# Kernel optimization log

Measured on AMD Instinct MI355X. Metric: run time of the kernel, lower is better.

Reference implementation:

```python
import jax, jax.numpy as jnp
import numpy as np

V, T, D, L, H, F = 32000, 1024, 768, 8, 12, 3072
DH = D // H
SCALE = 1.0 / np.sqrt(DH)
EPS = 1e-5


def layer_norm(x, w, b):
    mu = jnp.mean(x, axis=-1, keepdims=True)
    var = jnp.mean(jnp.square(x - mu), axis=-1, keepdims=True)
    return (x - mu) * jax.lax.rsqrt(var + EPS) * w + b


def setup_inputs() -> dict:
    key = jax.random.key(0)
    ks = jax.random.split(key, 10)
    def nrm(k, shape, std=0.02):
        return (jax.random.normal(k, shape, dtype=jnp.float32) * std)
    inp = {
        "idx": jax.random.randint(ks[0], (4, T), 0, V, dtype=jnp.int32),
        "targets": jax.random.randint(ks[1], (4, T), 0, V, dtype=jnp.int32),
        "tok_emb": nrm(ks[2], (V, D)),
        "pos_emb": nrm(ks[3], (T, D)),
        "qkv_w": nrm(ks[4], (L, 3 * D, D)),
        "qkv_b": jnp.zeros((L, 3 * D), jnp.float32),
        "proj_w": nrm(ks[5], (L, D, D)),
        "proj_b": jnp.zeros((L, D), jnp.float32),
        "fc1_w": nrm(ks[6], (L, F, D)),
        "fc1_b": jnp.zeros((L, F), jnp.float32),
        "fc2_w": nrm(ks[7], (L, D, F)),
        "fc2_b": jnp.zeros((L, D), jnp.float32),
        "ln1_w": jnp.ones((L, D), jnp.float32),
        "ln1_b": jnp.zeros((L, D), jnp.float32),
        "ln2_w": jnp.ones((L, D), jnp.float32),
        "ln2_b": jnp.zeros((L, D), jnp.float32),
        "lnf_w": jnp.ones((D,), jnp.float32),
        "lnf_b": jnp.zeros((D,), jnp.float32),
    }
    return inp


def gpt_forward(idx, targets, tok_emb, pos_emb, qkv_w, qkv_b, proj_w, proj_b,
                fc1_w, fc1_b, fc2_w, fc2_b, ln1_w, ln1_b, ln2_w, ln2_b, lnf_w, lnf_b):
    B, Tc = idx.shape
    x = tok_emb[idx] + pos_emb[:Tc][None]  # [B,T,D]
    causal = jnp.tril(jnp.ones((Tc, Tc), bool))

    def block(x, p):
        qw, qb, pw, pb, f1w, f1b, f2w, f2b, l1w, l1b, l2w, l2b = p
        h = layer_norm(x, l1w, l1b)
        qkv = h @ qw.T + qb  # [B,T,3D]
        q, k, v = jnp.split(qkv, 3, axis=-1)
        q = q.reshape(B, Tc, H, DH).transpose(0, 2, 1, 3)  # [B,H,T,DH]
        k = k.reshape(B, Tc, H, DH).transpose(0, 2, 1, 3)
        v = v.reshape(B, Tc, H, DH).transpose(0, 2, 1, 3)
        att = jnp.einsum('bhqd,bhkd->bhqk', q, k) * SCALE
        att = jnp.where(causal, att, -jnp.inf)
        att = jax.nn.softmax(att, axis=-1)
        y = jnp.einsum('bhqk,bhkd->bhqd', att, v)
        y = y.transpose(0, 2, 1, 3).reshape(B, Tc, D)
        x = x + y @ pw.T + pb
        h2 = layer_norm(x, l2w, l2b)
        x = x + jax.nn.gelu(h2 @ f1w.T + f1b, approximate=False) @ f2w.T + f2b
        return x, None

    x, _ = jax.lax.scan(block, x, (qkv_w, qkv_b, proj_w, proj_b,
                                   fc1_w, fc1_b, fc2_w, fc2_b,
                                   ln1_w, ln1_b, ln2_w, ln2_b))
    x = layer_norm(x, lnf_w, lnf_b)
    logits = jnp.einsum('btd,vd->btv', x, tok_emb)  # tied lm_head, output_mult=1
    logp = jax.nn.log_softmax(logits, axis=-1)
    valid = targets != -100
    tgt = jnp.where(valid, targets, 0)
    nll = -jnp.take_along_axis(logp, tgt[..., None], axis=-1)[..., 0]
    loss = jnp.sum(nll * valid) / jnp.maximum(jnp.sum(valid), 1)
    return logits, loss


def reference(idx, targets, tok_emb, pos_emb, qkv_w, qkv_b, proj_w, proj_b,
              fc1_w, fc1_b, fc2_w, fc2_b, ln1_w, ln1_b, ln2_w, ln2_b, lnf_w, lnf_b):
    return gpt_forward(idx, targets, tok_emb, pos_emb, qkv_w, qkv_b, proj_w, proj_b,
                       fc1_w, fc1_b, fc2_w, fc2_b, ln1_w, ln1_b, ln2_w, ln2_b, lnf_w, lnf_b)
```

## Files before the change

kernel.cpp:

```cpp
#include <hip/hip_runtime.h>
#include <hip/hip_bf16.h>
#include <math.h>

#define BATCH 4
#define T 1024
#define D 768
#define L 8
#define H 12
#define F 3072
#define V 32000
#define DH 64
#define M (BATCH*T)
#define D3 (3*D)
#define SCALE 0.125f
#define VCHUNK 6400
#define PBT 125

typedef unsigned short u16;
typedef __attribute__((ext_vector_type(8))) short bf16x8;
typedef __attribute__((ext_vector_type(4))) float f32x4;

__device__ inline u16 f2b(float f) {
  __hip_bfloat16 h = __float2bfloat16(f);
  return *(u16*)&h;
}

__device__ inline void gll16(const void* g, void* l) {
  __builtin_amdgcn_global_load_lds(
      (const __attribute__((address_space(1))) unsigned int*)g,
      (__attribute__((address_space(3))) unsigned int*)l, 16, 0, 0);
}

__device__ inline int swzi(int r, int c) {
  return (r * 64 + c) ^ ((((r & 7) ^ ((r >> 3) & 7))) << 3);
}

__device__ inline float block_reduce(float v, bool is_max, float* buf4) {
  int lane = threadIdx.x & 63, wid = threadIdx.x >> 6;
#pragma unroll
  for (int off = 32; off; off >>= 1) {
    float o = __shfl_down(v, off, 64);
    v = is_max ? fmaxf(v, o) : v + o;
  }
  if (lane == 0) buf4[wid] = v;
  __syncthreads();
  float r = is_max ? fmaxf(fmaxf(buf4[0], buf4[1]), fmaxf(buf4[2], buf4[3]))
                   : buf4[0] + buf4[1] + buf4[2] + buf4[3];
  __syncthreads();
  return r;
}

__global__ __launch_bounds__(256) void k_embed(const int* __restrict__ idx,
                                               const float* __restrict__ tok,
                                               const float* __restrict__ pos,
                                               float* __restrict__ x) {
  int i = blockIdx.x * 256 + threadIdx.x;
  int row = i / D, d = i - row * D;
  int t = row & (T - 1);
  x[i] = tok[(size_t)idx[row] * D + d] + pos[(size_t)t * D + d];
}

__global__ __launch_bounds__(256) void k_cvt(const float* __restrict__ in,
                                             u16* __restrict__ out, int n4) {
  int i = blockIdx.x * 256 + threadIdx.x;
  if (i >= n4) return;
  float4 v = ((const float4*)in)[i];
  ushort4 o;
  o.x = f2b(v.x); o.y = f2b(v.y); o.z = f2b(v.z); o.w = f2b(v.w);
  ((ushort4*)out)[i] = o;
}

__global__ __launch_bounds__(256) void k_cvtw(const float* __restrict__ q,
                                              const float* __restrict__ p,
                                              const float* __restrict__ f1,
                                              const float* __restrict__ f2,
                                              u16* __restrict__ out) {
  const int N0 = L * D3 * D / 4, N1 = L * D * D / 4;
  const int N2 = L * F * D / 4, N3 = L * D * F / 4;
  int i = blockIdx.x * 256 + threadIdx.x;
  if (i >= N0 + N1 + N2 + N3) return;
  const float* src;
  int j = i;
  if (i < N0) { src = q; }
  else if (i < N0 + N1) { src = p; j = i - N0; }
  else if (i < N0 + N1 + N2) { src = f1; j = i - N0 - N1; }
  else { src = f2; j = i - N0 - N1 - N2; }
  float4 v = ((const float4*)src)[j];
  ushort4 o;
  o.x = f2b(v.x); o.y = f2b(v.y); o.z = f2b(v.z); o.w = f2b(v.w);
  ((ushort4*)out)[i] = o;
}

__global__ __launch_bounds__(256) void k_lnorm(const float* __restrict__ x,
                                               const float* __restrict__ w,
                                               const float* __restrict__ b,
                                               u16* __restrict__ out) {
  int lane = threadIdx.x & 63, wid = threadIdx.x >> 6;
  int row = blockIdx.x * 4 + wid;
  const float4* xr = (const float4*)(x + (size_t)row * D);
  float4 v[3];
  float s = 0.f, ss = 0.f;
#pragma unroll
  for (int p = 0; p < 3; ++p) {
    v[p] = xr[lane + 64 * p];
    s += v[p].x + v[p].y + v[p].z + v[p].w;
    ss += v[p].x * v[p].x + v[p].y * v[p].y + v[p].z * v[p].z + v[p].w * v[p].w;
  }
#pragma unroll
  for (int off = 32; off; off >>= 1) {
    s += __shfl_xor(s, off, 64);
    ss += __shfl_xor(ss, off, 64);
  }
  float mu = s * (1.0f / D);
  float var = ss * (1.0f / D) - mu * mu;
  float rs = rsqrtf(var + 1e-5f);
  ushort4* orow = (ushort4*)(out + (size_t)row * D);
#pragma unroll
  for (int p = 0; p < 3; ++p) {
    float4 wv = ((const float4*)w)[lane + 64 * p];
    float4 bv = ((const float4*)b)[lane + 64 * p];
    ushort4 o;
    o.x = f2b((v[p].x - mu) * rs * wv.x + bv.x);
    o.y = f2b((v[p].y - mu) * rs * wv.y + bv.y);
    o.z = f2b((v[p].z - mu) * rs * wv.z + bv.z);
    o.w = f2b((v[p].w - mu) * rs * wv.w + bv.w);
    orow[lane + 64 * p] = o;
  }
}

__global__ __launch_bounds__(512, 2) void k_gemm8(
    const u16* __restrict__ A, const u16* __restrict__ W,
    const float* __restrict__ bias, const float* __restrict__ resid,
    void* __restrict__ Cout, int K, int ldC, int flags) {
  __shared__ __attribute__((aligned(16))) u16 lds[2][2][128 * 64];
  int tid = threadIdx.x, w = tid >> 6, lane = tid & 63;
  int wm = w >> 2, wn = w & 3;
  int bn = blockIdx.x, bm = blockIdx.y;
  int frow = lane & 15, g = lane >> 4;
  int sr = lane >> 3, scu = lane & 7;
  const u16* Ab = A + (size_t)bm * 128 * K;
  const u16* Wb = W + (size_t)bn * 128 * K;
  int NT = K >> 6;

  f32x4 acc[4][2];
#pragma unroll
  for (int i = 0; i < 4; ++i)
#pragma unroll
    for (int j = 0; j < 2; ++j) acc[i][j] = (f32x4)(0.f);

#define STG(t)                                                            \
  {                                                                       \
    _Pragma("unroll") for (int rr = 0; rr < 2; ++rr) {                    \
      int row = rr * 64 + w * 8 + sr;                                     \
      int gcu = scu ^ (row & 7);                                          \
      gll16(Ab + (size_t)row * K + (t) * 64 + gcu * 8,                    \
            &lds[(t) & 1][0][(rr * 64 + w * 8) * 64]);                    \
      gll16(Wb + (size_t)row * K + (t) * 64 + gcu * 8,                    \
            &lds[(t) & 1][1][(rr * 64 + w * 8) * 64]);                    \
    }                                                                     \
  }

  STG(0);
  asm volatile("s_waitcnt vmcnt(0)");
  __builtin_amdgcn_s_barrier();

  for (int t = 0; t < NT; ++t) {
    if (t + 1 < NT) {
      STG(t + 1);
      asm volatile("s_waitcnt vmcnt(4)");
    } else {
      asm volatile("s_waitcnt vmcnt(0)");
    }
    __builtin_amdgcn_s_barrier();
    const u16* bA = &lds[t & 1][0][0];
    const u16* bB = &lds[t & 1][1][0];
    bf16x8 ar[8], br[4];
#pragma unroll
    for (int i = 0; i < 4; ++i)
#pragma unroll
      for (int kk = 0; kk < 2; ++kk) {
        int r = wm * 64 + i * 16 + frow;
        ar[i * 2 + kk] = *(const bf16x8*)(bA + r * 64 + ((g + kk * 4) ^ (r & 7)) * 8);
      }
#pragma unroll
    for (int j = 0; j < 2; ++j)
#pragma unroll
      for (int kk = 0; kk < 2; ++kk) {
        int r = wn * 32 + j * 16 + frow;
        br[j * 2 + kk] = *(const bf16x8*)(bB + r * 64 + ((g + kk * 4) ^ (r & 7)) * 8);
      }
    __builtin_amdgcn_s_setprio(1);
#pragma unroll
    for (int i = 0; i < 4; ++i)
#pragma unroll
      for (int j = 0; j < 2; ++j)
#pragma unroll
        for (int kk = 0; kk < 2; ++kk)
          acc[i][j] = __builtin_amdgcn_mfma_f32_16x16x32_bf16(
              ar[i * 2 + kk], br[j * 2 + kk], acc[i][j], 0, 0, 0);
    __builtin_amdgcn_s_setprio(0);
    __builtin_amdgcn_s_barrier();
  }
#undef STG

  int m0 = bm * 128 + wm * 64 + g * 4;
  int n0 = bn * 128 + wn * 32 + frow;
#pragma unroll
  for (int i = 0; i < 4; ++i) {
#pragma unroll
    for (int j = 0; j < 2; ++j) {
      int n = n0 + j * 16;
      float bv = (flags & 1) ? bias[n] : 0.f;
#pragma unroll
      for (int q = 0; q < 4; ++q) {
        int m = m0 + i * 16 + q;
        size_t off = (size_t)m * ldC + n;
        float v = acc[i][j][q] + bv;
        if (flags & 4) v = 0.5f * v * (1.0f + erff(v * 0.70710678118f));
        if (flags & 2) v += resid[off];
        if (flags & 8) ((u16*)Cout)[off] = f2b(v);
        else           ((float*)Cout)[off] = v;
      }
    }
  }
}

__global__ __launch_bounds__(512, 2) void k_lm256(
    const u16* __restrict__ A,
    const u16* __restrict__ B,
    float* __restrict__ C,
    float* __restrict__ pm, float* __restrict__ ps,
    int gc0) {
  __shared__ __attribute__((aligned(16))) u16 lds[2][2][2][128 * 64];
  __shared__ float pml[256][4], psl[256][4];
  const int K = 768, NT = 12;
  int tid = threadIdx.x, w = tid >> 6, lane = tid & 63;
  int wm = w >> 2, wn = w & 3;
  int bm = blockIdx.x, bn = blockIdx.y;
  int frow = lane & 15, g = lane >> 4;
  int sr = lane >> 3, scu = lane & 7;
  const u16* Abase = A + (size_t)bm * 256 * K;
  const u16* Bbase = B + (size_t)bn * 256 * K;

  f32x4 acc[8][4];
#pragma unroll
  for (int i = 0; i < 8; ++i)
#pragma unroll
    for (int j = 0; j < 4; ++j) acc[i][j] = (f32x4)(0.f);

#define STAGE(t, h)                                                       \
  {                                                                       \
    const u16* src = ((h) < 2 ? Abase : Bbase) + (size_t)(((h)&1) * 128) * K; \
    u16* dst = &lds[(t) & 1][(h) >> 1][(h)&1][0];                         \
    _Pragma("unroll") for (int rr = 0; rr < 2; ++rr) {                    \
      int row = rr * 64 + w * 8 + sr;                                     \
      int gcu = scu ^ (row & 7);                                          \
      gll16(src + (size_t)row * K + (t) * 64 + gcu * 8,                   \
            dst + (rr * 64 + w * 8) * 64);                                \
    }                                                                     \
  }

  bf16x8 ar[8], br[8];
#define LDA(T_, ILO)                                                      \
  {                                                                       \
    const u16* base = &lds[(T_)&1][0][wm][0];                             \
    _Pragma("unroll") for (int ii = 0; ii < 4; ++ii)                      \
    _Pragma("unroll") for (int kk = 0; kk < 2; ++kk) {                    \
      int ri = ((ILO) + ii) * 16 + frow;                                  \
      int u = (g + kk * 4) ^ (ri & 7);                                    \
      ar[ii * 2 + kk] = *(const bf16x8*)(base + ri * 64 + u * 8);         \
    }                                                                     \
  }
#define LDB(T_, JLO, BO)                                                  \
  {                                                                       \
    const u16* base = &lds[(T_)&1][1][wn >> 1][0];                        \
    _Pragma("unroll") for (int jj = 0; jj < 2; ++jj)                      \
    _Pragma("unroll") for (int kk = 0; kk < 2; ++kk) {                    \
      int rj = (wn & 1) * 64 + ((JLO) + jj) * 16 + frow;                  \
      int u = (g + kk * 4) ^ (rj & 7);                                    \
      br[(BO) + jj * 2 + kk] = *(const bf16x8*)(base + rj * 64 + u * 8);  \
    }                                                                     \
  }
#define MFMA16(ILO, JLO, BO)                                              \
  _Pragma("unroll") for (int ii = 0; ii < 4; ++ii)                        \
  _Pragma("unroll") for (int jj = 0; jj < 2; ++jj)                        \
  _Pragma("unroll") for (int kk = 0; kk < 2; ++kk)                        \
    acc[(ILO) + ii][(JLO) + jj] = __builtin_amdgcn_mfma_f32_16x16x32_bf16( \
        ar[ii * 2 + kk], br[(BO) + jj * 2 + kk], acc[(ILO) + ii][(JLO) + jj], 0, 0, 0);

  STAGE(0, 0); STAGE(0, 1); STAGE(0, 2); STAGE(0, 3);
  asm volatile("s_waitcnt vmcnt(0)");
  __builtin_amdgcn_s_barrier();

  for (int t = 0; t < NT; ++t) {
    bool pf = (t + 1 < NT);
    LDA(t, 0); LDB(t, 0, 0);
    if (pf) { STAGE(t + 1, 0); STAGE(t + 1, 1); }
    __builtin_amdgcn_s_setprio(1);
    MFMA16(0, 0, 0);
    __builtin_amdgcn_s_setprio(0);
    __builtin_amdgcn_s_barrier();
    LDB(t, 2, 4);
    if (pf) { STAGE(t + 1, 2); STAGE(t + 1, 3); }
    __builtin_amdgcn_s_setprio(1);
    MFMA16(0, 2, 4);
    __builtin_amdgcn_s_setprio(0);
    __builtin_amdgcn_s_barrier();
    LDA(t, 4);
    __builtin_amdgcn_s_setprio(1);
    MFMA16(4, 2, 4);
    __builtin_amdgcn_s_setprio(0);
    __builtin_amdgcn_s_barrier();
    __builtin_amdgcn_s_setprio(1);
    MFMA16(4, 0, 0);
    __builtin_amdgcn_s_setprio(0);
    asm volatile("s_waitcnt vmcnt(0)");
    __builtin_amdgcn_s_barrier();
  }

#pragma unroll
  for (int ii = 0; ii < 8; ++ii) {
#pragma unroll
    for (int q = 0; q < 4; ++q) {
      float mx = fmaxf(fmaxf(acc[ii][0][q], acc[ii][1][q]),
                       fmaxf(acc[ii][2][q], acc[ii][3][q]));
      mx = fmaxf(mx, __shfl_xor(mx, 1, 64));
      mx = fmaxf(mx, __shfl_xor(mx, 2, 64));
      mx = fmaxf(mx, __shfl_xor(mx, 4, 64));
      mx = fmaxf(mx, __shfl_xor(mx, 8, 64));
      float sm = 0.f;
#pragma unroll
      for (int jj = 0; jj < 4; ++jj) sm += __expf(acc[ii][jj][q] - mx);
      sm += __shfl_xor(sm, 1, 64);
      sm += __shfl_xor(sm, 2, 64);
      sm += __shfl_xor(sm, 4, 64);
      sm += __shfl_xor(sm, 8, 64);
      int lrow = wm * 128 + ii * 16 + g * 4 + q;
      if (frow == 0) { pml[lrow][wn] = mx; psl[lrow][wn] = sm; }
      size_t off = (size_t)(bm * 256 + lrow) * V + gc0 + bn * 256 + wn * 64 + frow;
#pragma unroll
      for (int jj = 0; jj < 4; ++jj) C[off + jj * 16] = acc[ii][jj][q];
    }
  }
  __syncthreads();
  if (tid < 256) {
    float m = fmaxf(fmaxf(pml[tid][0], pml[tid][1]), fmaxf(pml[tid][2], pml[tid][3]));
    float s = 0.f;
#pragma unroll
    for (int w4 = 0; w4 < 4; ++w4) s += psl[tid][w4] * __expf(pml[tid][w4] - m);
    size_t grow = bm * 256 + tid;
    int pb = gc0 / 256 + bn;
    pm[grow * PBT + pb] = m;
    ps[grow * PBT + pb] = s;
  }
#undef STAGE
#undef LDA
#undef LDB
#undef MFMA16
}

__global__ __launch_bounds__(512) void k_fattn(const u16* __restrict__ qkv,
                                               u16* __restrict__ y) {
  __shared__ __attribute__((aligned(16))) u16 lQ[2][64 * 64];
  __shared__ __attribute__((aligned(16))) u16 lK[64 * 64];
  __shared__ __attribute__((aligned(16))) u16 lVt[64 * 64];
  __shared__ __attribute__((aligned(16))) u16 lP[128 * 64];
  int tid = threadIdx.x;
  int w = tid >> 6, lane = tid & 63;
  int tq = w >> 2, ws4 = w & 3;
  int xi = blockIdx.x;
  int bh = blockIdx.y, b = bh / H, h = bh - b * H;
  int myqt = tq ? xi : (15 - xi);
  const u16* base = qkv + (size_t)b * T * D3 + h * DH;
  int srow = lane >> 3;
  int scu = lane & 7;
  int frow = lane & 15, g = lane >> 4;
  int s16 = ws4 * 16;
  int qrow = g * 4;
  int f7 = frow & 7;

#pragma unroll
  for (int c = 0; c < 2; ++c) {
    int row = s16 + c * 8 + srow;
    int gcu = scu ^ (row & 7);
    gll16(base + (size_t)(myqt * 64 + row) * D3 + gcu * 8,
          &lQ[tq][(s16 + c * 8) * 64]);
  }

  float m_r[4], l_r[4];
  f32x4 o[4];
#pragma unroll
  for (int i = 0; i < 4; ++i) { m_r[i] = -1e30f; l_r[i] = 0.f; o[i] = (f32x4)(0.f); }

  int ktmax = 15 - xi;
  int kvrow = w * 8 + srow;
  uint4 kr = *(const uint4*)(base + D + (size_t)kvrow * D3 + scu * 8);
  uint4 vr = *(const uint4*)(base + 2 * D + (size_t)kvrow * D3 + scu * 8);

  for (int kt = 0; kt <= ktmax; ++kt) {
    __syncthreads();
    int k0 = kt * 64;
    *(uint4*)(lK + kvrow * 64 + (scu ^ (kvrow & 7)) * 8) = kr;
    {
      unsigned vals[4] = {vr.x, vr.y, vr.z, vr.w};
#pragma unroll
      for (int e = 0; e < 4; ++e) {
        lVt[swzi(scu * 8 + 2 * e, kvrow)]     = (u16)(vals[e] & 0xffff);
        lVt[swzi(scu * 8 + 2 * e + 1, kvrow)] = (u16)(vals[e] >> 16);
      }
    }
    __syncthreads();
    if (kt < ktmax) {
      int rown = k0 + 64 + kvrow;
      kr = *(const uint4*)(base + D + (size_t)rown * D3 + scu * 8);
      vr = *(const uint4*)(base + 2 * D + (size_t)rown * D3 + scu * 8);
    }

    if (tq == 0 || kt <= xi) {
      bool diag = (kt == myqt);
      const u16* lq = &lQ[tq][0];
      bf16x8 aq0 = *(const bf16x8*)(lq + (s16 + frow) * 64 + (g ^ f7) * 8);
      bf16x8 aq1 = *(const bf16x8*)(lq + (s16 + frow) * 64 + ((g + 4) ^ f7) * 8);
      f32x4 sv[4];
#pragma unroll
      for (int kn = 0; kn < 4; ++kn) {
        bf16x8 bk0 = *(const bf16x8*)(lK + (kn * 16 + frow) * 64 + (g ^ f7) * 8);
        bf16x8 bk1 = *(const bf16x8*)(lK + (kn * 16 + frow) * 64 + ((g + 4) ^ f7) * 8);
        sv[kn] = __builtin_amdgcn_mfma_f32_16x16x32_bf16(aq0, bk0, (f32x4)(0.f), 0, 0, 0);
        sv[kn] = __builtin_amdgcn_mfma_f32_16x16x32_bf16(aq1, bk1, sv[kn], 0, 0, 0);
      }
#pragma unroll
      for (int kn = 0; kn < 4; ++kn)
#pragma unroll
        for (int qi = 0; qi < 4; ++qi) {
          float v = sv[kn][qi] * SCALE;
          if (diag) {
            int qg = myqt * 64 + s16 + qrow + qi;
            int kg = k0 + kn * 16 + frow;
            if (kg > qg) v = -1e30f;
          }
          sv[kn][qi] = v;
        }
#pragma unroll
      for (int qi = 0; qi < 4; ++qi) {
        float rm = fmaxf(fmaxf(sv[0][qi], sv[1][qi]), fmaxf(sv[2][qi], sv[3][qi]));
        rm = fmaxf(rm, __shfl_xor(rm, 1, 64));
        rm = fmaxf(rm, __shfl_xor(rm, 2, 64));
        rm = fmaxf(rm, __shfl_xor(rm, 4, 64));
        rm = fmaxf(rm, __shfl_xor(rm, 8, 64));
        float mn = fmaxf(m_r[qi], rm);
        float alpha = __expf(m_r[qi] - mn);
        m_r[qi] = mn;
        float rs = 0.f;
#pragma unroll
        for (int kn = 0; kn < 4; ++kn) {
          float p = __expf(sv[kn][qi] - mn);
          sv[kn][qi] = p;
          rs += p;
        }
        rs += __shfl_xor(rs, 1, 64);
        rs += __shfl_xor(rs, 2, 64);
        rs += __shfl_xor(rs, 4, 64);
        rs += __shfl_xor(rs, 8, 64);
        l_r[qi] = l_r[qi] * alpha + rs;
#pragma unroll
        for (int df = 0; df < 4; ++df) o[df][qi] *= alpha;
      }
#pragma unroll
      for (int kn = 0; kn < 4; ++kn)
#pragma unroll
        for (int qi = 0; qi < 4; ++qi)
          lP[swzi(w * 16 + qrow + qi, kn * 16 + frow)] = f2b(sv[kn][qi]);
      bf16x8 pa0 = *(const bf16x8*)(lP + swzi(w * 16 + frow, g * 8));
      bf16x8 pa1 = *(const bf16x8*)(lP + swzi(w * 16 + frow, 32 + g * 8));
#pragma unroll
      for (int df = 0; df < 4; ++df) {
        bf16x8 bv0 = *(const bf16x8*)(lVt + swzi(df * 16 + frow, g * 8));
        bf16x8 bv1 = *(const bf16x8*)(lVt + swzi(df * 16 + frow, 32 + g * 8));
        o[df] = __builtin_amdgcn_mfma_f32_16x16x32_bf16(pa0, bv0, o[df], 0, 0, 0);
        o[df] = __builtin_amdgcn_mfma_f32_16x16x32_bf16(pa1, bv1, o[df], 0, 0, 0);
      }
    }
  }

#pragma unroll
  for (int df = 0; df < 4; ++df)
#pragma unroll
    for (int qi = 0; qi < 4; ++qi) {
      int qg = myqt * 64 + s16 + qrow + qi;
      y[(size_t)(b * T + qg) * D + h * DH + df * 16 + frow] =
          f2b(o[df][qi] / l_r[qi]);
    }
}

__global__ __launch_bounds__(256) void k_loss_rows(
    const float* __restrict__ pm, const float* __restrict__ ps,
    const float* __restrict__ logits, const int* __restrict__ targets,
    float* __restrict__ nll) {
  int lane = threadIdx.x & 63, wid = threadIdx.x >> 6;
  int row = blockIdx.x * 4 + wid;
  const float* pmr = pm + (size_t)row * PBT;
  const float* psr = ps + (size_t)row * PBT;
  float m = -1e30f;
  for (int i = lane; i < PBT; i += 64) m = fmaxf(m, pmr[i]);
#pragma unroll
  for (int off = 32; off; off >>= 1) m = fmaxf(m, __shfl_xor(m, off, 64));
  float s = 0.f;
  for (int i = lane; i < PBT; i += 64) s += psr[i] * __expf(pmr[i] - m);
#pragma unroll
  for (int off = 32; off; off >>= 1) s += __shfl_xor(s, off, 64);
  if (lane == 0) {
    int tgt = targets[row];
    nll[row] = (tgt != -100) ? (m + logf(s) - logits[(size_t)row * V + tgt]) : 0.f;
  }
}

__global__ __launch_bounds__(256) void k_loss_final(const float* __restrict__ nll,
                                                    const int* __restrict__ targets,
                                                    float* __restrict__ out) {
  __shared__ float buf4[4];
  float s = 0.f, c = 0.f;
  for (int i = threadIdx.x; i < M; i += 256) {
    s += nll[i];
    c += (targets[i] != -100) ? 1.f : 0.f;
  }
  s = block_reduce(s, false, buf4);
  c = block_reduce(c, false, buf4);
  if (threadIdx.x == 0) out[0] = s / fmaxf(c, 1.f);
}

extern "C" void kernel_launch(void* const* d_in, const int* in_sizes, int n_in,
                              void* d_out, int out_size, void* d_ws, size_t ws_size,
                              hipStream_t stream) {
  const int* idx       = (const int*)d_in[0];
  const int* targets   = (const int*)d_in[1];
  const float* tok     = (const float*)d_in[2];
  const float* pos     = (const float*)d_in[3];
  const float* qkv_w   = (const float*)d_in[4];
  const float* qkv_b   = (const float*)d_in[5];
  const float* proj_w  = (const float*)d_in[6];
  const float* proj_b  = (const float*)d_in[7];
  const float* fc1_w   = (const float*)d_in[8];
  const float* fc1_b   = (const float*)d_in[9];
  const float* fc2_w   = (const float*)d_in[10];
  const float* fc2_b   = (const float*)d_in[11];
  const float* ln1_w   = (const float*)d_in[12];
  const float* ln1_b   = (const float*)d_in[13];
  const float* ln2_w   = (const float*)d_in[14];
  const float* ln2_b   = (const float*)d_in[15];
  const float* lnf_w   = (const float*)d_in[16];
  const float* lnf_b   = (const float*)d_in[17];

  float* logits = (float*)d_out;

  char* ws = (char*)d_ws;
  float* x   = (float*)ws;
  u16* hb    = (u16*)(ws + 12582912);
  u16* yb    = (u16*)(ws + 18874368);
  u16* wb    = (u16*)(ws + 25165824);
  bool big = ws_size >= (size_t)(25165824 + 49152000 + 2048000 * 2 + 16384);
  float* pm, * ps, * nll;
  if (big) {
    pm  = (float*)(ws + 25165824 + 49152000);
    ps  = (float*)(ws + 25165824 + 49152000 + 2048000);
    nll = (float*)(ws + 25165824 + 49152000 + 4096000);
  } else {
    pm  = (float*)(ws + 34996224);
    ps  = (float*)(ws + 37044224);
    nll = (float*)(ws + 39092224);
  }

  u16* qkvb   = (u16*)logits;
  u16* f1b    = (u16*)(logits + 9437184);
  u16* wqkv   = (u16*)(logits + 15728640);
  u16* wproj  = (u16*)(logits + 22806528);
  u16* wfc1   = (u16*)(logits + 25165824);
  u16* wfc2   = (u16*)(logits + 34603008);

  {
    const int NW4 = (L * D3 * D + L * D * D + L * F * D + L * D * F) / 4;
    k_cvtw<<<(NW4 + 255) / 256, 256, 0, stream>>>(qkv_w, proj_w, fc1_w, fc2_w, wqkv);
  }

  k_embed<<<(M * D) / 256, 256, 0, stream>>>(idx, tok, pos, x);

  for (int l = 0; l < L; ++l) {
    k_lnorm<<<M / 4, 256, 0, stream>>>(x, ln1_w + (size_t)l * D, ln1_b + (size_t)l * D, hb);
    k_gemm8<<<dim3(D3 / 128, M / 128), 512, 0, stream>>>(
        hb, wqkv + (size_t)l * D3 * D, qkv_b + (size_t)l * D3, nullptr, qkvb, D, D3, 9);
    k_fattn<<<dim3(8, BATCH * H), 512, 0, stream>>>(qkvb, yb);
    k_gemm8<<<dim3(D / 128, M / 128), 512, 0, stream>>>(
        yb, wproj + (size_t)l * D * D, proj_b + (size_t)l * D, x, x, D, D, 3);
    k_lnorm<<<M / 4, 256, 0, stream>>>(x, ln2_w + (size_t)l * D, ln2_b + (size_t)l * D, hb);
    k_gemm8<<<dim3(F / 128, M / 128), 512, 0, stream>>>(
        hb, wfc1 + (size_t)l * F * D, fc1_b + (size_t)l * F, nullptr, f1b, D, F, 13);
    k_gemm8<<<dim3(D / 128, M / 128), 512, 0, stream>>>(
        f1b, wfc2 + (size_t)l * D * F, fc2_b + (size_t)l * D, x, x, F, D, 3);
  }

  k_lnorm<<<M / 4, 256, 0, stream>>>(x, lnf_w, lnf_b, hb);
  if (big) {
    k_cvt<<<(V * D / 4 + 255) / 256, 256, 0, stream>>>(tok, wb, V * D / 4);
    k_lm256<<<dim3(M / 256, V / 256), 512, 0, stream>>>(
        hb, wb, logits, pm, ps, 0);
  } else {
    for (int c = 0; c < 5; ++c) {
      k_cvt<<<(VCHUNK * D / 4 + 255) / 256, 256, 0, stream>>>(
          tok + (size_t)c * VCHUNK * D, wb, VCHUNK * D / 4);
      k_lm256<<<dim3(M / 256, VCHUNK / 256), 512, 0, stream>>>(
          hb, wb, logits, pm, ps, c * VCHUNK);
    }
  }
  k_loss_rows<<<M / 4, 256, 0, stream>>>(pm, ps, logits, targets, nll);
  k_loss_final<<<1, 256, 0, stream>>>(nll, targets, logits + (size_t)M * V);
}
```

Baseline: 1.917 ms.

## Split-K fc2 GEMM with partial-sum fused LayerNorm; switch LM head to 128 tiles

The fc2 GEMM (K=3072, only 6x32 output tiles) is now split four ways along K through a grid z dimension, and each split writes fp32 partials into a scratch area inside the logits buffer. A new kernel sums the partials, bias and residual into x and applies the next LayerNorm in one pass. The aim is better CU occupancy for the small-N GEMM. The LM head also moves from 256x256 tiles to 128x128 tiles with twice as many partial softmax stats per row. The cost is extra fp32 partial traffic, plus a larger workspace needed to take the big path.

Measured after the change: 1.983 ms. +3.5%, slower.

```diff
diff --git a/kernel.cpp b/kernel.cpp
--- a/kernel.cpp
+++ b/kernel.cpp
@@ -15,6 +15,7 @@
 #define SCALE 0.125f
 #define VCHUNK 6400
 #define PBT 125
+#define PBT2 250
 
 typedef unsigned short u16;
 typedef __attribute__((ext_vector_type(8))) short bf16x8;
@@ -128,19 +129,165 @@
   }
 }
 
+__global__ __launch_bounds__(256) void k_lncomb(float* __restrict__ x,
+                                                const float* __restrict__ parts,
+                                                const float* __restrict__ bias2,
+                                                const float* __restrict__ w,
+                                                const float* __restrict__ b,
+                                                u16* __restrict__ out) {
+  int lane = threadIdx.x & 63, wid = threadIdx.x >> 6;
+  int row = blockIdx.x * 4 + wid;
+  float4* xr = (float4*)(x + (size_t)row * D);
+  float4 v[3];
+  float s = 0.f, ss = 0.f;
+#pragma unroll
+  for (int p = 0; p < 3; ++p) {
+    v[p] = xr[lane + 64 * p];
+#pragma unroll
+    for (int pp = 0; pp < 4; ++pp) {
+      float4 pv = ((const float4*)(parts + (size_t)pp * M * D + (size_t)row * D))[lane + 64 * p];
+      v[p].x += pv.x; v[p].y += pv.y; v[p].z += pv.z; v[p].w += pv.w;
+    }
+    float4 b2 = ((const float4*)bias2)[lane + 64 * p];
+    v[p].x += b2.x; v[p].y += b2.y; v[p].z += b2.z; v[p].w += b2.w;
+    s += v[p].x + v[p].y + v[p].z + v[p].w;
+    ss += v[p].x * v[p].x + v[p].y * v[p].y + v[p].z * v[p].z + v[p].w * v[p].w;
+  }
+#pragma unroll
+  for (int off = 32; off; off >>= 1) {
+    s += __shfl_xor(s, off, 64);
+    ss += __shfl_xor(ss, off, 64);
+  }
+  float mu = s * (1.0f / D);
+  float var = ss * (1.0f / D) - mu * mu;
+  float rs = rsqrtf(var + 1e-5f);
+  ushort4* orow = (ushort4*)(out + (size_t)row * D);
+#pragma unroll
+  for (int p = 0; p < 3; ++p) {
+    xr[lane + 64 * p] = v[p];
+    float4 wv = ((const float4*)w)[lane + 64 * p];
+    float4 bv = ((const float4*)b)[lane + 64 * p];
+    ushort4 o;
+    o.x = f2b((v[p].x - mu) * rs * wv.x + bv.x);
+    o.y = f2b((v[p].y - mu) * rs * wv.y + bv.y);
+    o.z = f2b((v[p].z - mu) * rs * wv.z + bv.z);
+    o.w = f2b((v[p].w - mu) * rs * wv.w + bv.w);
+    orow[lane + 64 * p] = o;
+  }
+}
+
 __global__ __launch_bounds__(512, 2) void k_gemm8(
     const u16* __restrict__ A, const u16* __restrict__ W,
     const float* __restrict__ bias, const float* __restrict__ resid,
-    void* __restrict__ Cout, int K, int ldC, int flags) {
+    void* __restrict__ Cout, int kLen, int kStride, int ldC, int flags) {
   __shared__ __attribute__((aligned(16))) u16 lds[2][2][128 * 64];
   int tid = threadIdx.x, w = tid >> 6, lane = tid & 63;
   int wm = w >> 2, wn = w & 3;
   int bn = blockIdx.x, bm = blockIdx.y;
   int frow = lane & 15, g = lane >> 4;
   int sr = lane >> 3, scu = lane & 7;
+  int kz = (flags & 16) ? blockIdx.z * kLen : 0;
+  const u16* Ab = A + (size_t)bm * 128 * kStride + kz;
+  const u16* Wb = W + (size_t)bn * 128 * kStride + kz;
+  float* Cp = (float*)Cout + ((flags & 16) ? (size_t)blockIdx.z * M * (size_t)ldC : 0);
+  int NT = kLen >> 6;
+
+  f32x4 acc[4][2];
+#pragma unroll
+  for (int i = 0; i < 4; ++i)
+#pragma unroll
+    for (int j = 0; j < 2; ++j) acc[i][j] = (f32x4)(0.f);
+
+#define STG(t)                                                            \
+  {                                                                       \
+    _Pragma("unroll") for (int rr = 0; rr < 2; ++rr) {                    \
+      int row = rr * 64 + w * 8 + sr;                                     \
+      int gcu = scu ^ (row & 7);                                          \
+      gll16(Ab + (size_t)row * kStride + (t) * 64 + gcu * 8,              \
+            &lds[(t) & 1][0][(rr * 64 + w * 8) * 64]);                    \
+      gll16(Wb + (size_t)row * kStride + (t) * 64 + gcu * 8,              \
+            &lds[(t) & 1][1][(rr * 64 + w * 8) * 64]);                    \
+    }                                                                     \
+  }
+
+  STG(0);
+  asm volatile("s_waitcnt vmcnt(0)");
+  __builtin_amdgcn_s_barrier();
+
+  for (int t = 0; t < NT; ++t) {
+    if (t + 1 < NT) {
+      STG(t + 1);
+      asm volatile("s_waitcnt vmcnt(4)");
+    } else {
+      asm volatile("s_waitcnt vmcnt(0)");
+    }
+    __builtin_amdgcn_s_barrier();
+    const u16* bA = &lds[t & 1][0][0];
+    const u16* bB = &lds[t & 1][1][0];
+    bf16x8 ar[8], br[4];
+#pragma unroll
+    for (int i = 0; i < 4; ++i)
+#pragma unroll
+      for (int kk = 0; kk < 2; ++kk) {
+        int r = wm * 64 + i * 16 + frow;
+        ar[i * 2 + kk] = *(const bf16x8*)(bA + r * 64 + ((g + kk * 4) ^ (r & 7)) * 8);
+      }
+#pragma unroll
+    for (int j = 0; j < 2; ++j)
+#pragma unroll
+      for (int kk = 0; kk < 2; ++kk) {
+        int r = wn * 32 + j * 16 + frow;
+        br[j * 2 + kk] = *(const bf16x8*)(bB + r * 64 + ((g + kk * 4) ^ (r & 7)) * 8);
+      }
+    __builtin_amdgcn_s_setprio(1);
+#pragma unroll
+    for (int i = 0; i < 4; ++i)
+#pragma unroll
+      for (int j = 0; j < 2; ++j)
+#pragma unroll
+        for (int kk = 0; kk < 2; ++kk)
+          acc[i][j] = __builtin_amdgcn_mfma_f32_16x16x32_bf16(
+              ar[i * 2 + kk], br[j * 2 + kk], acc[i][j], 0, 0, 0);
+    __builtin_amdgcn_s_setprio(0);
+    __builtin_amdgcn_s_barrier();
+  }
+#undef STG
+
+  int m0 = bm * 128 + wm * 64 + g * 4;
+  int n0 = bn * 128 + wn * 32 + frow;
+#pragma unroll
+  for (int i = 0; i < 4; ++i) {
+#pragma unroll
+    for (int j = 0; j < 2; ++j) {
+      int n = n0 + j * 16;
+      float bv = (flags & 1) ? bias[n] : 0.f;
+#pragma unroll
+      for (int q = 0; q < 4; ++q) {
+        int m = m0 + i * 16 + q;
+        size_t off = (size_t)m * ldC + n;
+        float v = acc[i][j][q] + bv;
+        if (flags & 4) v = 0.5f * v * (1.0f + erff(v * 0.70710678118f));
+        if (flags & 2) v += resid[off];
+        if (flags & 8) ((u16*)Cout)[off] = f2b(v);
+        else           Cp[off] = v;
+      }
+    }
+  }
+}
+
+__global__ __launch_bounds__(512, 2) void k_lm128(
+    const u16* __restrict__ A, const u16* __restrict__ B,
+    float* __restrict__ C, float* __restrict__ pm, float* __restrict__ ps) {
+  __shared__ __attribute__((aligned(16))) u16 lds[2][2][128 * 64];
+  __shared__ float pml[128][4], psl[128][4];
+  const int K = 768, NT = 12;
+  int tid = threadIdx.x, w = tid >> 6, lane = tid & 63;
+  int wm = w >> 2, wn = w & 3;
+  int bm = blockIdx.x, bn = blockIdx.y;
+  int frow = lane & 15, g = lane >> 4;
+  int sr = lane >> 3, scu = lane & 7;
   const u16* Ab = A + (size_t)bm * 128 * K;
-  const u16* Wb = W + (size_t)bn * 128 * K;
-  int NT = K >> 6;
+  const u16* Bb = B + (size_t)bn * 128 * K;
 
   f32x4 acc[4][2];
 #pragma unroll
@@ -155,7 +302,7 @@
       int gcu = scu ^ (row & 7);                                          \
       gll16(Ab + (size_t)row * K + (t) * 64 + gcu * 8,                    \
             &lds[(t) & 1][0][(rr * 64 + w * 8) * 64]);                    \
-      gll16(Wb + (size_t)row * K + (t) * 64 + gcu * 8,                    \
+      gll16(Bb + (size_t)row * K + (t) * 64 + gcu * 8,                    \
             &lds[(t) & 1][1][(rr * 64 + w * 8) * 64]);                    \
     }                                                                     \
   }
@@ -203,33 +350,43 @@
   }
 #undef STG
 
-  int m0 = bm * 128 + wm * 64 + g * 4;
   int n0 = bn * 128 + wn * 32 + frow;
 #pragma unroll
   for (int i = 0; i < 4; ++i) {
 #pragma unroll
-    for (int j = 0; j < 2; ++j) {
-      int n = n0 + j * 16;
-      float bv = (flags & 1) ? bias[n] : 0.f;
-#pragma unroll
-      for (int q = 0; q < 4; ++q) {
-        int m = m0 + i * 16 + q;
-        size_t off = (size_t)m * ldC + n;
-        float v = acc[i][j][q] + bv;
-        if (flags & 4) v = 0.5f * v * (1.0f + erff(v * 0.70710678118f));
-        if (flags & 2) v += resid[off];
-        if (flags & 8) ((u16*)Cout)[off] = f2b(v);
-        else           ((float*)Cout)[off] = v;
-      }
-    }
+    for (int q = 0; q < 4; ++q) {
+      int lrow = wm * 64 + i * 16 + g * 4 + q;
+      size_t off = (size_t)(bm * 128 + lrow) * V + n0;
+      C[off]      = acc[i][0][q];
+      C[off + 16] = acc[i][1][q];
+      float mx = fmaxf(acc[i][0][q], acc[i][1][q]);
+      mx = fmaxf(mx, __shfl_xor(mx, 1, 64));
+      mx = fmaxf(mx, __shfl_xor(mx, 2, 64));
+      mx = fmaxf(mx, __shfl_xor(mx, 4, 64));
+      mx = fmaxf(mx, __shfl_xor(mx, 8, 64));
+      float sm = __expf(acc[i][0][q] - mx) + __expf(acc[i][1][q] - mx);
+      sm += __shfl_xor(sm, 1, 64);
+      sm += __shfl_xor(sm, 2, 64);
+      sm += __shfl_xor(sm, 4, 64);
+      sm += __shfl_xor(sm, 8, 64);
+      if (frow == 0) { pml[lrow][wn] = mx; psl[lrow][wn] = sm; }
+    }
+  }
+  __syncthreads();
+  if (tid < 128) {
+    float m = fmaxf(fmaxf(pml[tid][0], pml[tid][1]), fmaxf(pml[tid][2], pml[tid][3]));
+    float s = 0.f;
+#pragma unroll
+    for (int w4 = 0; w4 < 4; ++w4) s += psl[tid][w4] * __expf(pml[tid][w4] - m);
+    size_t grow = bm * 128 + tid;
+    pm[grow * PBT2 + bn] = m;
+    ps[grow * PBT2 + bn] = s;
   }
 }
 
 __global__ __launch_bounds__(512, 2) void k_lm256(
-    const u16* __restrict__ A,
-    const u16* __restrict__ B,
-    float* __restrict__ C,
-    float* __restrict__ pm, float* __restrict__ ps,
+    const u16* __restrict__ A, const u16* __restrict__ B,
+    float* __restrict__ C, float* __restrict__ pm, float* __restrict__ ps,
     int gc0) {
   __shared__ __attribute__((aligned(16))) u16 lds[2][2][2][128 * 64];
   __shared__ float pml[256][4], psl[256][4];
@@ -496,17 +653,17 @@
 __global__ __launch_bounds__(256) void k_loss_rows(
     const float* __restrict__ pm, const float* __restrict__ ps,
     const float* __restrict__ logits, const int* __restrict__ targets,
-    float* __restrict__ nll) {
+    float* __restrict__ nll, int pbt) {
   int lane = threadIdx.x & 63, wid = threadIdx.x >> 6;
   int row = blockIdx.x * 4 + wid;
-  const float* pmr = pm + (size_t)row * PBT;
-  const float* psr = ps + (size_t)row * PBT;
+  const float* pmr = pm + (size_t)row * pbt;
+  const float* psr = ps + (size_t)row * pbt;
   float m = -1e30f;
-  for (int i = lane; i < PBT; i += 64) m = fmaxf(m, pmr[i]);
+  for (int i = lane; i < pbt; i += 64) m = fmaxf(m, pmr[i]);
 #pragma unroll
   for (int off = 32; off; off >>= 1) m = fmaxf(m, __shfl_xor(m, off, 64));
   float s = 0.f;
-  for (int i = lane; i < PBT; i += 64) s += psr[i] * __expf(pmr[i] - m);
+  for (int i = lane; i < pbt; i += 64) s += psr[i] * __expf(pmr[i] - m);
 #pragma unroll
   for (int off = 32; off; off >>= 1) s += __shfl_xor(s, off, 64);
   if (lane == 0) {
@@ -558,12 +715,12 @@
   u16* hb    = (u16*)(ws + 12582912);
   u16* yb    = (u16*)(ws + 18874368);
   u16* wb    = (u16*)(ws + 25165824);
-  bool big = ws_size >= (size_t)(25165824 + 49152000 + 2048000 * 2 + 16384);
+  bool big = ws_size >= (size_t)(25165824 + 49152000 + 4096000 * 2 + 16384);
   float* pm, * ps, * nll;
   if (big) {
     pm  = (float*)(ws + 25165824 + 49152000);
-    ps  = (float*)(ws + 25165824 + 49152000 + 2048000);
-    nll = (float*)(ws + 25165824 + 49152000 + 4096000);
+    ps  = (float*)(ws + 25165824 + 49152000 + 4096000);
+    nll = (float*)(ws + 25165824 + 49152000 + 8192000);
   } else {
     pm  = (float*)(ws + 34996224);
     ps  = (float*)(ws + 37044224);
@@ -576,6 +733,7 @@
   u16* wproj  = (u16*)(logits + 22806528);
   u16* wfc1   = (u16*)(logits + 25165824);
   u16* wfc2   = (u16*)(logits + 34603008);
+  float* fc2p = (float*)((char*)logits + 201326592);
 
   {
     const int NW4 = (L * D3 * D + L * D * D + L * F * D + L * D * F) / 4;
@@ -585,24 +743,29 @@
   k_embed<<<(M * D) / 256, 256, 0, stream>>>(idx, tok, pos, x);
 
   for (int l = 0; l < L; ++l) {
-    k_lnorm<<<M / 4, 256, 0, stream>>>(x, ln1_w + (size_t)l * D, ln1_b + (size_t)l * D, hb);
+    if (l == 0)
+      k_lnorm<<<M / 4, 256, 0, stream>>>(x, ln1_w, ln1_b, hb);
+    else
+      k_lncomb<<<M / 4, 256, 0, stream>>>(x, fc2p, fc2_b + (size_t)(l - 1) * D,
+                                          ln1_w + (size_t)l * D, ln1_b + (size_t)l * D, hb);
     k_gemm8<<<dim3(D3 / 128, M / 128), 512, 0, stream>>>(
-        hb, wqkv + (size_t)l * D3 * D, qkv_b + (size_t)l * D3, nullptr, qkvb, D, D3, 9);
+        hb, wqkv + (size_t)l * D3 * D, qkv_b + (size_t)l * D3, nullptr, qkvb, D, D, D3, 9);
     k_fattn<<<dim3(8, BATCH * H), 512, 0, stream>>>(qkvb, yb);
     k_gemm8<<<dim3(D / 128, M / 128), 512, 0, stream>>>(
-        yb, wproj + (size_t)l * D * D, proj_b + (size_t)l * D, x, x, D, D, 3);
+        yb, wproj + (size_t)l * D * D, proj_b + (size_t)l * D, x, x, D, D, D, 3);
     k_lnorm<<<M / 4, 256, 0, stream>>>(x, ln2_w + (size_t)l * D, ln2_b + (size_t)l * D, hb);
     k_gemm8<<<dim3(F / 128, M / 128), 512, 0, stream>>>(
-        hb, wfc1 + (size_t)l * F * D, fc1_b + (size_t)l * F, nullptr, f1b, D, F, 13);
-    k_gemm8<<<dim3(D / 128, M / 128), 512, 0, stream>>>(
-        f1b, wfc2 + (size_t)l * D * F, fc2_b + (size_t)l * D, x, x, F, D, 3);
-  }
-
-  k_lnorm<<<M / 4, 256, 0, stream>>>(x, lnf_w, lnf_b, hb);
+        hb, wfc1 + (size_t)l * F * D, fc1_b + (size_t)l * F, nullptr, f1b, D, D, F, 13);
+    k_gemm8<<<dim3(D / 128, M / 128, 4), 512, 0, stream>>>(
+        f1b, wfc2 + (size_t)l * D * F, nullptr, nullptr, fc2p, 768, F, D, 16);
+  }
+
+  k_lncomb<<<M / 4, 256, 0, stream>>>(x, fc2p, fc2_b + (size_t)(L - 1) * D,
+                                      lnf_w, lnf_b, hb);
   if (big) {
     k_cvt<<<(V * D / 4 + 255) / 256, 256, 0, stream>>>(tok, wb, V * D / 4);
-    k_lm256<<<dim3(M / 256, V / 256), 512, 0, stream>>>(
-        hb, wb, logits, pm, ps, 0);
+    k_lm128<<<dim3(M / 128, V / 128), 512, 0, stream>>>(hb, wb, logits, pm, ps);
+    k_loss_rows<<<M / 4, 256, 0, stream>>>(pm, ps, logits, targets, nll, PBT2);
   } else {
     for (int c = 0; c < 5; ++c) {
       k_cvt<<<(VCHUNK * D / 4 + 255) / 256, 256, 0, stream>>>(
@@ -610,7 +773,7 @@
       k_lm256<<<dim3(M / 256, VCHUNK / 256), 512, 0, stream>>>(
           hb, wb, logits, pm, ps, c * VCHUNK);
     }
-  }
-  k_loss_rows<<<M / 4, 256, 0, stream>>>(pm, ps, logits, targets, nll);
+    k_loss_rows<<<M / 4, 256, 0, stream>>>(pm, ps, logits, targets, nll, PBT);
+  }
   k_loss_final<<<1, 256, 0, stream>>>(nll, targets, logits + (size_t)M * V);
 }
```
